# Performance work log

Measured on AMD Instinct MI355X. Metric: run time of the kernel, lower is better.

The kernel has to match this reference:

```python
import jax, jax.numpy as jnp
import numpy as np
from jax import lax

Z_MAX = 0.3
WAVELENGTHS = jnp.array([0.65, 0.53, 0.47], jnp.float32)
LUMA = jnp.array([0.299, 0.587, 0.114], jnp.float32)


def conv2d(x, w, b):
    # x: (B,C,H,W), w: (O,I,kh,kw), SAME padding, stride 1
    y = lax.conv_general_dilated(x, w, (1, 1), 'SAME',
                                 dimension_numbers=('NCHW', 'OIHW', 'NCHW'))
    return y + b[None, :, None, None]


def group_norm(x, g, b, eps=1e-5):
    # GroupNorm(num_groups=1): normalize over (C,H,W) per sample
    mu = x.mean(axis=(1, 2, 3), keepdims=True)
    var = ((x - mu) ** 2).mean(axis=(1, 2, 3), keepdims=True)
    xn = (x - mu) * lax.rsqrt(var + eps)
    return xn * g[None, :, None, None] + b[None, :, None, None]


def setup_inputs() -> dict:
    key = jax.random.key(0)
    ks = jax.random.split(key, 16)
    B, C, H, W = 8, 3, 512, 512
    PH, ZH, MH = 16, 16, 32
    s = 0.1
    inp = {
        'x': jax.random.uniform(ks[0], (B, C, H, W), jnp.float32),
        'norm_g': jnp.ones((C,), jnp.float32), 'norm_b': jnp.zeros((C,), jnp.float32),
        'ph_w1': jax.random.normal(ks[1], (PH, C, 3, 3), jnp.float32) * s,
        'ph_b1': jnp.zeros((PH,), jnp.float32),
        'ph_w2': jax.random.normal(ks[2], (C, PH, 3, 3), jnp.float32) * s,
        'ph_b2': jnp.zeros((C,), jnp.float32),
        'z_w1': jax.random.normal(ks[3], (ZH, C, 3, 3), jnp.float32) * s,
        'z_b1': jnp.zeros((ZH,), jnp.float32),
        'z_w2': jax.random.normal(ks[4], (C, ZH, 3, 3), jnp.float32) * s,
        'z_b2': jnp.zeros((C,), jnp.float32),
        'freq_gain': jax.random.normal(ks[5], (C,), jnp.float32) * 0.01,
        'mix_w1': jax.random.normal(ks[6], (MH, C + 2, 3, 3), jnp.float32) * s,
        'mix_b1': jnp.zeros((MH,), jnp.float32),
        'gn1_g': jnp.ones((MH,), jnp.float32), 'gn1_b': jnp.zeros((MH,), jnp.float32),
        'mix_w2': jax.random.normal(ks[7], (MH, MH, 3, 3), jnp.float32) * s,
        'mix_b2': jnp.zeros((MH,), jnp.float32),
        'gn2_g': jnp.ones((MH,), jnp.float32), 'gn2_b': jnp.zeros((MH,), jnp.float32),
        'mix_w3': jax.random.normal(ks[8], (C, MH, 1, 1), jnp.float32) * s,
        'mix_b3': jnp.zeros((C,), jnp.float32),
        'se_w1': jax.random.normal(ks[9], (4, C), jnp.float32) * s,   # mid = max(3//4,4)=4
        'se_b1': jnp.zeros((4,), jnp.float32),
        'se_w2': jax.random.normal(ks[10], (C, 4), jnp.float32) * s,
        'se_b2': jnp.zeros((C,), jnp.float32),
        'alpha': jnp.asarray(0.3, jnp.float32),
    }
    return inp


def reference(x, norm_g, norm_b, ph_w1, ph_b1, ph_w2, ph_b2,
              z_w1, z_b1, z_w2, z_b2, freq_gain,
              mix_w1, mix_b1, gn1_g, gn1_b, mix_w2, mix_b2, gn2_g, gn2_b,
              mix_w3, mix_b3, se_w1, se_b1, se_w2, se_b2, alpha):
    B, C, H, W = x.shape
    # 1) norm
    xn = group_norm(x, norm_g, norm_b)
    # 2) phase prediction (small CNN, phi in [-pi, pi])
    h = jax.nn.silu(conv2d(xn, ph_w1, ph_b1))
    phi = jnp.tanh(conv2d(h, ph_w2, ph_b2)) * jnp.pi
    # 3) per-pixel propagation distance z in [0, z_max]
    hz = jax.nn.silu(conv2d(xn, z_w1, z_b1))
    z = jax.nn.sigmoid(conv2d(hz, z_w2, z_b2)) * Z_MAX
    # 4) complex field U0 = amp * exp(i*phi)  (amp_mode='identity')
    U0 = lax.complex(x * jnp.cos(phi), x * jnp.sin(phi))
    # 5) ASM propagation. kz = 2*pi*sqrt(1/lam^2 - fx^2 - fy^2), per-channel wavelength.
    fy = jnp.fft.fftfreq(H).astype(jnp.float32)
    fx = jnp.fft.fftfreq(W).astype(jnp.float32)
    f2 = fy[:, None] ** 2 + fx[None, :] ** 2                     # (H,W)
    inv_l2 = (1.0 / WAVELENGTHS ** 2)[:, None, None]             # (3,1,1)
    kz = 2.0 * jnp.pi * jnp.sqrt(jnp.maximum(inv_l2 - f2[None], 0.0))  # (3,H,W)
    # spatially varying z: base propagation at mean z + spatial phase correction
    z_mean = z.mean(axis=(2, 3), keepdims=True)                  # (B,3,1,1)
    Uf = jnp.fft.fft2(U0)
    Uf = Uf * (1.0 + freq_gain)[None, :, None, None].astype(Uf.dtype)  # FreqEnhance gain
    hp = kz[None] * z_mean                                       # (B,3,H,W)
    Uz = jnp.fft.ifft2(Uf * lax.complex(jnp.cos(hp), jnp.sin(hp)))
    k0 = (2.0 * jnp.pi / WAVELENGTHS)[None, :, None, None]
    cp = k0 * (z - z_mean)
    Uz = Uz * lax.complex(jnp.cos(cp), jnp.sin(cp))
    # 6) J = |Uz| with clamped sqrt
    J = jnp.sqrt(jnp.maximum(Uz.real ** 2 + Uz.imag ** 2, 1e-12))
    # 7) mix head: [x, J_luma, J_contrast] -> delta
    lw = LUMA[None, :, None, None]
    x_l = (x * lw).sum(axis=1, keepdims=True)
    J_l = (J * lw).sum(axis=1, keepdims=True)
    mix_in = jnp.concatenate([x, J_l, J_l - x_l], axis=1)        # (B,5,H,W)
    d = jax.nn.silu(group_norm(conv2d(mix_in, mix_w1, mix_b1), gn1_g, gn1_b))
    d = jax.nn.silu(group_norm(conv2d(d, mix_w2, mix_b2), gn2_g, gn2_b))
    delta = conv2d(d, mix_w3, mix_b3)                            # (B,3,H,W)
    # 8) SE channel attention
    p = delta.mean(axis=(2, 3))                                  # (B,3)
    wse = jax.nn.sigmoid(jax.nn.silu(p @ se_w1.T + se_b1) @ se_w2.T + se_b2)
    delta = delta * wse[:, :, None, None]
    # 9) residual update
    return x + alpha * delta
```

## Files before the change

### kernel.cpp

```cpp
#include <hip/hip_runtime.h>
#include <hip/hip_bf16.h>
#include <math.h>

#define DINL __device__ __forceinline__

namespace {
constexpr int Bn = 8, Cn = 3, Hn = 512, Wn = 512;
constexpr int HW  = Hn * Wn;
constexpr int CHW = Cn * HW;
constexpr float GEPS = 1e-5f;
constexpr float PIf  = 3.14159265358979323846f;

constexpr size_t OFF_RED = 0;
constexpr size_t OFF_PHI = 512;
constexpr size_t OFF_U   = OFF_PHI + (size_t)Bn * CHW * 2;
constexpr size_t OFF_J   = OFF_U   + (size_t)Bn * CHW * 4;
constexpr size_t OFF_D   = OFF_J   + (size_t)Bn * CHW * 2;
constexpr size_t OFF_Y2  = OFF_D   + (size_t)Bn * CHW * 2;
constexpr size_t OFF_W1B = OFF_Y2  + (size_t)Bn * 32 * HW;
constexpr size_t OFF_W2F = OFF_W1B + 3072 * 2;
constexpr size_t OFF_WH1 = OFF_W2F + 9216;
constexpr size_t OFF_WP2 = OFF_WH1 + 4608 * 2;
constexpr size_t OFF_WZ2 = OFF_WP2 + 4608;
constexpr size_t OFF_PRM = OFF_WZ2 + 4608;
constexpr size_t OFF_PART= OFF_PRM + 160 * 4;
constexpr int PZ = 0;
constexpr int PG1 = 24576;
constexpr int PG2 = 40960;
constexpr int PD  = 57344;
}

typedef __bf16 bfx8 __attribute__((ext_vector_type(8)));
typedef float  fx4  __attribute__((ext_vector_type(4)));

DINL float frcp(float a) { return __builtin_amdgcn_rcpf(a); }
DINL float sigm(float a) { return frcp(1.f + __expf(-a)); }
DINL float siluf(float a) { return a * frcp(1.f + __expf(-a)); }
DINL float ftanh(float a) { return 1.f - 2.f * frcp(1.f + __expf(2.f * a)); }
DINL unsigned short f2bf(float f) {
    unsigned u = __float_as_uint(f);
    return (unsigned short)((u + 0x7FFFu + ((u >> 16) & 1u)) >> 16);
}
DINL float bf2f(unsigned short h) {
    return __uint_as_float(((unsigned)h) << 16);
}
DINL unsigned short t1(float a) { return (unsigned short)(__float_as_uint(a) >> 16); }
DINL unsigned t2(float a, float b) {
    return (__float_as_uint(a) >> 16) | (__float_as_uint(b) & 0xFFFF0000u);
}
DINL unsigned char f2f8(float v) {
    return (unsigned char)(__builtin_amdgcn_cvt_pk_fp8_f32(v, v, 0, false) & 0xFF);
}
DINL unsigned short pk8(float a, float b) {
    return (unsigned short)(__builtin_amdgcn_cvt_pk_fp8_f32(a, b, 0, false) & 0xFFFF);
}
template<int SEL>
DINL float f8f(unsigned u) { return __builtin_amdgcn_cvt_f32_fp8(u, SEL); }
DINL unsigned pkh(float a, float b) {
    auto h = __builtin_amdgcn_cvt_pkrtz(a, b);
    unsigned u; __builtin_memcpy(&u, &h, 4); return u;
}
DINL float2 uph(unsigned u) {
    _Float16 h[2]; __builtin_memcpy(h, &u, 4);
    return make_float2((float)h[0], (float)h[1]);
}
DINL unsigned short f2h(float a) {
    _Float16 h = (_Float16)a; unsigned short s; __builtin_memcpy(&s, &h, 2); return s;
}
DINL float h2f(unsigned short s) {
    _Float16 h; __builtin_memcpy(&h, &s, 2); return (float)h;
}

DINL float blockReduceSum(float v) {
    __shared__ float sm[4];
    int lane = threadIdx.x & 63, wid = threadIdx.x >> 6;
    #pragma unroll
    for (int o = 32; o > 0; o >>= 1) v += __shfl_down(v, o, 64);
    __syncthreads();
    if (lane == 0) sm[wid] = v;
    __syncthreads();
    if (wid == 0) {
        float r = (lane < 4) ? sm[lane] : 0.f;
        r += __shfl_down(r, 2, 64);
        r += __shfl_down(r, 1, 64);
        return r;
    }
    return 0.f;
}

__global__ void k_zero(float* __restrict__ red) { red[threadIdx.x] = 0.f; }

__global__ __launch_bounds__(256) void k_red(const float* __restrict__ src,
                                             float* __restrict__ dst)
{
    const float4* s4 = (const float4*)(src + (size_t)blockIdx.x * 1024);
    float4 q = s4[threadIdx.x];
    float r = blockReduceSum(q.x + q.y + q.z + q.w);
    if (threadIdx.x == 0) dst[blockIdx.x] = r;
}

__global__ __launch_bounds__(256) void k_prep(
    const float* __restrict__ w1, const float* __restrict__ w2,
    const float* __restrict__ phw1, const float* __restrict__ zw1,
    const float* __restrict__ phw2, const float* __restrict__ zw2,
    const float* __restrict__ g2g, const float* __restrict__ g2b,
    const float* __restrict__ w3,
    unsigned short* __restrict__ w1bf, unsigned char* __restrict__ w2f8,
    unsigned short* __restrict__ wh1, unsigned char* __restrict__ wp2,
    unsigned char* __restrict__ wz2, float* __restrict__ prm)
{
    int i = blockIdx.x * 256 + threadIdx.x;
    if (i < 3072) {
        int o = i / 96, k = i - o * 96;
        int ky = k >> 5, r = k & 31, kx = r >> 3, c = r & 7;
        float v = (kx < 3 && c < 5) ? w1[o * 45 + c * 9 + ky * 3 + kx] : 0.f;
        w1bf[i] = f2bf(v);
    }
    if (i < 9216) {
        int tap = i >> 10, rr = i & 1023, o = rr >> 5, ci = rr & 31;
        w2f8[i] = f2f8(w2[o * 288 + ci * 9 + tap]);
    }
    if (i < 4608) {
        int o = i / 96, k = i - o * 96;
        int ky = k >> 5, r = k & 31, kx = r >> 3, c = r & 7;
        float v = 0.f;
        if (kx < 3 && c < 3)
            v = (o < 16) ? phw1[o * 27 + c * 9 + ky * 3 + kx]
                         : zw1[(o - 16) * 27 + c * 9 + ky * 3 + kx];
        wh1[i] = f2bf(v);
    }
    if (i < 4608) {
        int tap = i / 512, rr = i - tap * 512, n = rr >> 5, k = rr & 31;
        float vp = (n < 3 && k < 16) ? phw2[n * 144 + k * 9 + tap] : 0.f;
        float vz = (n < 3) ? zw2[n * 288 + k * 9 + tap] : 0.f;
        wp2[i] = f2f8(vp);
        wz2[i] = f2f8(vz);
    }
    if (i < 160) {
        if (i < 32) {
            int ch = (i & 1) * 16 + (i >> 1);
            prm[i] = g2g[ch];
        } else if (i < 64) {
            int j = i - 32, ch = (j & 1) * 16 + (j >> 1);
            prm[i] = g2b[ch];
        } else {
            int j = (i - 64) & 31, c = (i - 64) >> 5;
            int ch = (j & 1) * 16 + (j >> 1);
            prm[i] = w3[c * 32 + ch];
        }
    }
}

__global__ __launch_bounds__(256) void k_reduce_x(const float* __restrict__ x,
                                                  float* __restrict__ red) {
    int b = blockIdx.x >> 5, blk = blockIdx.x & 31;
    const float4* xv = (const float4*)(x + (size_t)b * CHW + (size_t)blk * (CHW / 32));
    float s = 0.f, ss = 0.f;
    for (int i = threadIdx.x; i < (CHW / 32) / 4; i += 256) {
        float4 v = xv[i];
        s  += v.x + v.y + v.z + v.w;
        ss += v.x * v.x + v.y * v.y + v.z * v.z + v.w * v.w;
    }
    float rs = blockReduceSum(s);
    float rss = blockReduceSum(ss);
    if (threadIdx.x == 0) { atomicAdd(&red[b], rs); atomicAdd(&red[8 + b], rss); }
}

__global__ __launch_bounds__(256) void k_heads(
    const float* __restrict__ x, const float* __restrict__ red,
    const float* __restrict__ ng, const float* __restrict__ nb,
    const unsigned short* __restrict__ wh1,
    const float* __restrict__ phb1, const float* __restrict__ zb1,
    const unsigned char* __restrict__ wp2, const unsigned char* __restrict__ wz2,
    const float* __restrict__ phb2, const float* __restrict__ zb2,
    unsigned short* __restrict__ phi, float* __restrict__ part)
{
    const int tx0 = blockIdx.x * 16, ty0 = blockIdx.y * 16, b = blockIdx.z;
    const int local = blockIdx.y * 32 + blockIdx.x;
    const bool edge = (blockIdx.x == 0) || (blockIdx.x == 31) ||
                      (blockIdx.y == 0) || (blockIdx.y == 31);
    __shared__ unsigned short mt8[20 * 21 * 8];
    __shared__ __attribute__((aligned(16))) unsigned char ht8[324 * 48];
    const int t = threadIdx.x;
    const float mu = red[b] * (1.f / CHW);
    const float rsv = rsqrtf(red[8 + b] * (1.f / CHW) - mu * mu + GEPS);
    float sc[3], sh[3];
    #pragma unroll
    for (int c = 0; c < 3; ++c) { sc[c] = rsv * ng[c]; sh[c] = nb[c] - mu * rsv * ng[c]; }
    if (edge) {
        for (int e = t; e < 20 * 21; e += 256) {
            int yy = e / 21, xx = e - yy * 21;
            int gy = ty0 - 2 + yy, gx = tx0 - 2 + xx;
            float v0 = 0, v1 = 0, v2 = 0;
            if (xx < 20 && (unsigned)gy < (unsigned)Hn && (unsigned)gx < (unsigned)Wn) {
                size_t p = (size_t)b * CHW + (size_t)gy * Wn + gx;
                v0 = x[p] * sc[0] + sh[0];
                v1 = x[p + HW] * sc[1] + sh[1];
                v2 = x[p + 2 * HW] * sc[2] + sh[2];
            }
            *(uint4*)(mt8 + e * 8) = make_uint4(t2(v0, v1), (unsigned)t1(v2), 0u, 0u);
        }
    } else {
        for (int e = t; e < 20 * 21; e += 256) {
            int yy = e / 21, xx = e - yy * 21;
            float v0 = 0, v1 = 0, v2 = 0;
            if (xx < 20) {
                size_t p = (size_t)b * CHW + (size_t)(ty0 - 2 + yy) * Wn + (tx0 - 2 + xx);
                v0 = x[p] * sc[0] + sh[0];
                v1 = x[p + HW] * sc[1] + sh[1];
                v2 = x[p + 2 * HW] * sc[2] + sh[2];
            }
            *(uint4*)(mt8 + e * 8) = make_uint4(t2(v0, v1), (unsigned)t1(v2), 0u, 0u);
        }
    }
    const int wv = t >> 6, lane = t & 63, ln = lane & 15, q = lane >> 4;
    bfx8 Bf[3][3];
    #pragma unroll
    for (int ks = 0; ks < 3; ++ks)
        #pragma unroll
        for (int nt = 0; nt < 3; ++nt)
            Bf[ks][nt] = *(const bfx8*)(wh1 + (nt * 16 + ln) * 96 + ks * 32 + q * 8);
    const float bb0 = phb1[ln], bb1 = zb1[ln], bb2 = zb1[16 + ln];
    __syncthreads();
    for (int mt = wv; mt < 21; mt += 4) {
        int p = mt * 16 + ln; if (p > 323) p = 323;
        const int hy = p / 18, hx = p - hy * 18;
        fx4 a0 = {0,0,0,0}, a1 = {0,0,0,0}, a2 = {0,0,0,0};
        #pragma unroll
        for (int ks = 0; ks < 3; ++ks) {
            bfx8 A = *(const bfx8*)(mt8 + ((hy + ks) * 21 + hx + q) * 8);
            a0 = __builtin_amdgcn_mfma_f32_16x16x32_bf16(A, Bf[ks][0], a0, 0, 0, 0);
            a1 = __builtin_amdgcn_mfma_f32_16x16x32_bf16(A, Bf[ks][1], a1, 0, 0, 0);
            a2 = __builtin_amdgcn_mfma_f32_16x16x32_bf16(A, Bf[ks][2], a2, 0, 0, 0);
        }
        const int prb = mt * 16 + q * 4;
        if (edge) {
            #pragma unroll
            for (int r = 0; r < 4; ++r) {
                const int pr = prb + r;
                if (pr < 324) {
                    const int py = pr / 18, px = pr - py * 18;
                    const int gy = ty0 - 1 + py, gx = tx0 - 1 + px;
                    const bool inimg = (unsigned)gy < (unsigned)Hn && (unsigned)gx < (unsigned)Wn;
                    unsigned char* hp = ht8 + pr * 48;
                    hp[ln]      = inimg ? f2f8(siluf(a0[r] + bb0)) : (unsigned char)0;
                    hp[16 + ln] = inimg ? f2f8(siluf(a1[r] + bb1)) : (unsigned char)0;
                    hp[32 + ln] = inimg ? f2f8(siluf(a2[r] + bb2)) : (unsigned char)0;
                }
            }
        } else {
            #pragma unroll
            for (int r = 0; r < 4; ++r) {
                const int pr = prb + r;
                if (pr < 324) {
                    unsigned char* hp = ht8 + pr * 48;
                    hp[ln]      = f2f8(siluf(a0[r] + bb0));
                    hp[16 + ln] = f2f8(siluf(a1[r] + bb1));
                    hp[32 + ln] = f2f8(siluf(a2[r] + bb2));
                }
            }
        }
    }
    __syncthreads();
    fx4 accp[4], accz[4];
    #pragma unroll
    for (int i = 0; i < 4; ++i) { accp[i] = fx4{0,0,0,0}; accz[i] = fx4{0,0,0,0}; }
    #pragma unroll
    for (int tap = 0; tap < 9; ++tap) {
        const int ky = tap / 3, kx = tap - ky * 3;
        long Bp = *(const long*)(wp2 + tap * 512 + ln * 32 + q * 8);
        long Bz = *(const long*)(wz2 + tap * 512 + ln * 32 + q * 8);
        #pragma unroll
        for (int i = 0; i < 4; ++i) {
            const int oy = wv * 4 + i;
            const unsigned char* ap = ht8 + ((oy + ky) * 18 + ln + kx) * 48;
            long Ap = *(const long*)(ap + q * 8);
            long Az = *(const long*)(ap + 16 + q * 8);
            accp[i] = __builtin_amdgcn_mfma_f32_16x16x32_fp8_fp8(Ap, Bp, accp[i], 0, 0, 0);
            accz[i] = __builtin_amdgcn_mfma_f32_16x16x32_fp8_fp8(Az, Bz, accz[i], 0, 0, 0);
        }
    }
    __syncthreads();
    float* phs = (float*)ht8;
    float* zs  = phs + 1024;
    if (ln < 3) {
        #pragma unroll
        for (int i = 0; i < 4; ++i)
            #pragma unroll
            for (int r = 0; r < 4; ++r) {
                int pl = (wv * 4 + i) * 16 + q * 4 + r;
                phs[pl * 4 + ln] = accp[i][r];
                zs [pl * 4 + ln] = accz[i][r];
            }
    }
    asm volatile("" ::: "memory");
    float4 pv = ((const float4*)phs)[t];
    float4 zv = ((const float4*)zs)[t];
    const int gy = ty0 + (t >> 4), gx = tx0 + (t & 15);
    size_t pp = (size_t)b * CHW + (size_t)gy * Wn + gx;
    phi[pp]          = f2h(ftanh(pv.x + phb2[0]) * PIf);
    phi[pp + HW]     = f2h(ftanh(pv.y + phb2[1]) * PIf);
    phi[pp + 2 * HW] = f2h(ftanh(pv.z + phb2[2]) * PIf);
    float z0 = sigm(zv.x + zb2[0]) * 0.3f;
    float z1 = sigm(zv.y + zb2[1]) * 0.3f;
    float z2 = sigm(zv.z + zb2[2]) * 0.3f;
    float r0 = blockReduceSum(z0);
    float r1 = blockReduceSum(z1);
    float r2 = blockReduceSum(z2);
    if (t == 0) {
        part[PZ + (size_t)(b * 3 + 0) * 1024 + local] = r0;
        part[PZ + (size_t)(b * 3 + 1) * 1024 + local] = r1;
        part[PZ + (size_t)(b * 3 + 2) * 1024 + local] = r2;
    }
}

template<bool INV>
DINL float2* fft512_wave4(float2* a, float2* b, const float2* tw, int l)
{
    float2* src = a; float2* dst = b;
    int s = 1;
    #pragma unroll
    for (int st = 0; st < 4; ++st) {
        #pragma unroll
        for (int h = 0; h < 2; ++h) {
            const int i = l + h * 64;
            const int q = i & (s - 1);
            const int sm = i - q;
            float2 A = src[i], B = src[i + 128], C = src[i + 256], D = src[i + 384];
            float t0x = A.x + C.x, t0y = A.y + C.y;
            float t1x = A.x - C.x, t1y = A.y - C.y;
            float t2x = B.x + D.x, t2y = B.y + D.y;
            float t3x = B.x - D.x, t3y = B.y - D.y;
            float i3x = INV ? -t3y : t3y;
            float i3y = INV ? t3x : -t3x;
            float u0x = t0x + t2x, u0y = t0y + t2y;
            float u2x = t0x - t2x, u2y = t0y - t2y;
            float u1x = t1x + i3x, u1y = t1y + i3y;
            float u3x = t1x - i3x, u3y = t1y - i3y;
            float2 w1 = tw[sm], w2 = tw[2 * sm], w3 = tw[3 * sm];
            float w1y = INV ? -w1.y : w1.y;
            float w2y = INV ? -w2.y : w2.y;
            float w3y = INV ? -w3.y : w3.y;
            const int base = q + 4 * sm;
            dst[base]         = make_float2(u0x, u0y);
            dst[base + s]     = make_float2(u1x * w1.x - u1y * w1y, u1x * w1y + u1y * w1.x);
            dst[base + 2 * s] = make_float2(u2x * w2.x - u2y * w2y, u2x * w2y + u2y * w2.x);
            dst[base + 3 * s] = make_float2(u3x * w3.x - u3y * w3y, u3x * w3y + u3y * w3.x);
        }
        float2* tmp = src; src = dst; dst = tmp;
        s <<= 2;
        asm volatile("" ::: "memory");
    }
    #pragma unroll
    for (int h = 0; h < 4; ++h) {
        const int j = l + h * 64;
        float2 u = src[j], v = src[j + 256];
        dst[j]       = make_float2(u.x + v.x, u.y + v.y);
        dst[j + 256] = make_float2(u.x - v.x, u.y - v.y);
    }
    float2* tmp = src; src = dst; dst = tmp;
    asm volatile("" ::: "memory");
    return src;
}

__global__ __launch_bounds__(256) void k_fftA(
    const float* __restrict__ x, const unsigned short* __restrict__ phi,
    unsigned* __restrict__ U)
{
    __shared__ float2 buf[4][2][512];
    __shared__ float2 tw[512];
    const int t = threadIdx.x, wv = t >> 6, l = t & 63;
    #pragma unroll
    for (int i = t; i < 512; i += 256) {
        float s, c; __sincosf(-2.f * PIf * (float)i * (1.f / 512.f), &s, &c);
        tw[i] = make_float2(c, s);
    }
    __syncthreads();
    const size_t line = (size_t)blockIdx.x * 4 + wv;
    const float* xr = x + line * 512;
    const unsigned short* pr = phi + line * 512;
    float2* A = buf[wv][0];
    float2* B = buf[wv][1];
    #pragma unroll
    for (int i = l; i < 512; i += 64) {
        float s, c; __sincosf(h2f(pr[i]), &s, &c);
        float xv = xr[i];
        A[i] = make_float2(xv * c, xv * s);
    }
    asm volatile("" ::: "memory");
    float2* res = fft512_wave4<false>(A, B, tw, l);
    unsigned* Ur = U + line * 512;
    #pragma unroll
    for (int i = l; i < 512; i += 64) Ur[i] = pkh(res[i].x, res[i].y);
}

__global__ __launch_bounds__(256) void k_transpose(unsigned* __restrict__ U)
{
    const int img = blockIdx.y;
    int rem = blockIdx.x, ti = 0;
    while (rem >= 16 - ti) { rem -= 16 - ti; ++ti; }
    const int tj = ti + rem;
    unsigned* Ub = U + (size_t)img * HW;
    __shared__ unsigned ta[32][33];
    __shared__ unsigned tb[32][33];
    const int t = threadIdx.x;
    const int cc = t & 31, r0 = t >> 5;
    const int ar = ti * 32, ac = tj * 32;
    #pragma unroll
    for (int k = 0; k < 4; ++k) {
        int r = r0 + k * 8;
        ta[r][cc] = Ub[(size_t)(ar + r) * 512 + ac + cc];
    }
    if (ti != tj) {
        #pragma unroll
        for (int k = 0; k < 4; ++k) {
            int r = r0 + k * 8;
            tb[r][cc] = Ub[(size_t)(ac + r) * 512 + ar + cc];
        }
    }
    __syncthreads();
    #pragma unroll
    for (int k = 0; k < 4; ++k) {
        int r = r0 + k * 8;
        Ub[(size_t)(ac + r) * 512 + ar + cc] = ta[cc][r];
    }
    if (ti != tj) {
        #pragma unroll
        for (int k = 0; k < 4; ++k) {
            int r = r0 + k * 8;
            Ub[(size_t)(ar + r) * 512 + ac + cc] = tb[cc][r];
        }
    }
}

__global__ __launch_bounds__(256) void k_fftB(
    unsigned* __restrict__ U, const float* __restrict__ red, const float* __restrict__ fgain)
{
    __shared__ float2 buf[4][2][512];
    __shared__ float2 tw[512];
    const int t = threadIdx.x, wv = t >> 6, l = t & 63;
    #pragma unroll
    for (int i = t; i < 512; i += 256) {
        float s, c; __sincosf(-2.f * PIf * (float)i * (1.f / 512.f), &s, &c);
        tw[i] = make_float2(c, s);
    }
    __syncthreads();
    const int line = blockIdx.x * 4 + wv;
    const int bc = line >> 9;
    const int fw = line & 511;
    const int c = bc % 3;
    unsigned* Ur = U + (size_t)line * 512;
    float2* A = buf[wv][0];
    float2* B = buf[wv][1];
    #pragma unroll
    for (int i = l; i < 512; i += 64) A[i] = uph(Ur[i]);
    asm volatile("" ::: "memory");
    float2* res = fft512_wave4<false>(A, B, tw, l);
    const float zm   = red[16 + bc] * (1.f / HW);
    const float gain = 1.f + fgain[c];
    const float lam  = (c == 0) ? 0.65f : (c == 1) ? 0.53f : 0.47f;
    const float il2  = 1.f / (lam * lam);
    const float fwv  = (float)(fw < 256 ? fw : fw - 512) * (1.f / 512.f);
    const float f2w  = fwv * fwv;
    #pragma unroll
    for (int i = l; i < 512; i += 64) {
        float fh = (float)(i < 256 ? i : i - 512) * (1.f / 512.f);
        float kz = 2.f * PIf * sqrtf(fmaxf(il2 - f2w - fh * fh, 0.f));
        float sn, cs; __sincosf(kz * zm, &sn, &cs);
        float2 v = res[i];
        res[i] = make_float2(gain * (v.x * cs - v.y * sn), gain * (v.x * sn + v.y * cs));
    }
    asm volatile("" ::: "memory");
    float2* other = (res == A) ? B : A;
    float2* res2 = fft512_wave4<true>(res, other, tw, l);
    #pragma unroll
    for (int i = l; i < 512; i += 64) {
        float2 v = res2[i];
        Ur[i] = pkh(v.x * (1.f / 512.f), v.y * (1.f / 512.f));
    }
}

__global__ __launch_bounds__(256) void k_fftC(
    const unsigned* __restrict__ U, unsigned short* __restrict__ J)
{
    __shared__ float2 buf[4][2][512];
    __shared__ float2 tw[512];
    const int t = threadIdx.x, wv = t >> 6, l = t & 63;
    #pragma unroll
    for (int i = t; i < 512; i += 256) {
        float s, c; __sincosf(-2.f * PIf * (float)i * (1.f / 512.f), &s, &c);
        tw[i] = make_float2(c, s);
    }
    __syncthreads();
    const size_t line = (size_t)blockIdx.x * 4 + wv;
    const unsigned* Ur = U + line * 512;
    float2* A = buf[wv][0];
    float2* B = buf[wv][1];
    #pragma unroll
    for (int i = l; i < 512; i += 64) A[i] = uph(Ur[i]);
    asm volatile("" ::: "memory");
    float2* res = fft512_wave4<true>(A, B, tw, l);
    unsigned short* Jr = J + line * 512;
    #pragma unroll
    for (int i = l; i < 512; i += 64) {
        float2 v = res[i];
        float re = v.x * (1.f / 512.f), im = v.y * (1.f / 512.f);
        Jr[i] = f2h(sqrtf(fmaxf(re * re + im * im, 1e-12f)));
    }
}

__global__ __launch_bounds__(256) void k_m1(
    const float* __restrict__ x, const unsigned short* __restrict__ Jb,
    const unsigned short* __restrict__ w1bf, const float* __restrict__ b1,
    float* __restrict__ part)
{
    const int tx0 = blockIdx.x * 16, ty0 = blockIdx.y * 16, b = blockIdx.z;
    const int local = blockIdx.y * 32 + blockIdx.x;
    const bool edge = (blockIdx.x == 0) || (blockIdx.x == 31) ||
                      (blockIdx.y == 0) || (blockIdx.y == 31);
    __shared__ unsigned short mt8[18 * 19 * 8];
    const int t = threadIdx.x;
    for (int e = t; e < 18 * 19; e += 256) {
        int yy = e / 19, xx = e - yy * 19;
        int gy = ty0 - 1 + yy, gx = tx0 - 1 + xx;
        float v0 = 0, v1 = 0, v2 = 0, jl = 0, d5 = 0;
        bool ok = edge ? (xx < 18 && (unsigned)gy < (unsigned)Hn && (unsigned)gx < (unsigned)Wn)
                       : (xx < 18);
        if (ok) {
            size_t p = (size_t)b * CHW + (size_t)gy * Wn + gx;
            v0 = x[p]; v1 = x[p + HW]; v2 = x[p + 2 * HW];
            float j0 = h2f(Jb[p]), j1 = h2f(Jb[p + HW]), j2 = h2f(Jb[p + 2 * HW]);
            float xl = 0.299f * v0 + 0.587f * v1 + 0.114f * v2;
            jl = 0.299f * j0 + 0.587f * j1 + 0.114f * j2;
            d5 = jl - xl;
        }
        *(uint4*)(mt8 + e * 8) = make_uint4(t2(v0, v1), t2(v2, jl), (unsigned)t1(d5), 0u);
    }
    __syncthreads();
    const int wv = t >> 6, lane = t & 63, ln = lane & 15, q = lane >> 4;
    bfx8 Bf[3][2];
    #pragma unroll
    for (int ks = 0; ks < 3; ++ks)
        #pragma unroll
        for (int nt = 0; nt < 2; ++nt)
            Bf[ks][nt] = *(const bfx8*)(w1bf + (nt * 16 + ln) * 96 + ks * 32 + q * 8);
    const float b1v0 = b1[ln], b1v1 = b1[16 + ln];
    float s = 0.f, ss = 0.f;
    #pragma unroll
    for (int i = 0; i < 4; ++i) {
        const int oy = wv * 4 + i;
        fx4 a0 = {0.f, 0.f, 0.f, 0.f}, a1 = {0.f, 0.f, 0.f, 0.f};
        #pragma unroll
        for (int ks = 0; ks < 3; ++ks) {
            bfx8 A = *(const bfx8*)(mt8 + ((oy + ks) * 19 + ln + q) * 8);
            a0 = __builtin_amdgcn_mfma_f32_16x16x32_bf16(A, Bf[ks][0], a0, 0, 0, 0);
            a1 = __builtin_amdgcn_mfma_f32_16x16x32_bf16(A, Bf[ks][1], a1, 0, 0, 0);
        }
        #pragma unroll
        for (int r = 0; r < 4; ++r) {
            float u0 = a0[r] + b1v0, u1 = a1[r] + b1v1;
            s += u0 + u1; ss += u0 * u0 + u1 * u1;
        }
    }
    float rs = blockReduceSum(s);
    float rss = blockReduceSum(ss);
    if (t == 0) {
        part[PG1 + (size_t)b * 1024 + local] = rs;
        part[PG1 + (size_t)(8 + b) * 1024 + local] = rss;
    }
}

__global__ __launch_bounds__(256) void k_m2(
    const float* __restrict__ x, const unsigned short* __restrict__ Jb,
    const unsigned short* __restrict__ w1bf, const float* __restrict__ b1,
    const float* __restrict__ g1g, const float* __restrict__ g1b,
    const unsigned char* __restrict__ w2f8, const float* __restrict__ b2,
    const float* __restrict__ red, float* __restrict__ part,
    unsigned char* __restrict__ y2)
{
    const int tx0 = blockIdx.x * 16, ty0 = blockIdx.y * 16, b = blockIdx.z;
    const int local = blockIdx.y * 32 + blockIdx.x;
    const bool edge = (blockIdx.x == 0) || (blockIdx.x == 31) ||
                      (blockIdx.y == 0) || (blockIdx.y == 31);
    __shared__ unsigned short mt8[20 * 21 * 8];
    __shared__ __attribute__((aligned(16))) unsigned char dt2[324 * 40];
    const int t = threadIdx.x;
    const float mu1 = red[40 + b] * (1.f / (32.f * HW));
    const float rs1 = rsqrtf(red[48 + b] * (1.f / (32.f * HW)) - mu1 * mu1 + GEPS);
    for (int e = t; e < 20 * 21; e += 256) {
        int yy = e / 21, xx = e - yy * 21;
        int gy = ty0 - 2 + yy, gx = tx0 - 2 + xx;
        float v0 = 0, v1 = 0, v2 = 0, jl = 0, d5 = 0;
        bool ok = edge ? (xx < 20 && (unsigned)gy < (unsigned)Hn && (unsigned)gx < (unsigned)Wn)
                       : (xx < 20);
        if (ok) {
            size_t p = (size_t)b * CHW + (size_t)gy * Wn + gx;
            v0 = x[p]; v1 = x[p + HW]; v2 = x[p + 2 * HW];
            float j0 = h2f(Jb[p]), j1 = h2f(Jb[p + HW]), j2 = h2f(Jb[p + 2 * HW]);
            float xl = 0.299f * v0 + 0.587f * v1 + 0.114f * v2;
            jl = 0.299f * j0 + 0.587f * j1 + 0.114f * j2;
            d5 = jl - xl;
        }
        *(uint4*)(mt8 + e * 8) = make_uint4(t2(v0, v1), t2(v2, jl), (unsigned)t1(d5), 0u);
    }
    const int wv = t >> 6, lane = t & 63, ln = lane & 15, q = lane >> 4;
    const float sc0 = rs1 * g1g[ln],       sc1 = rs1 * g1g[16 + ln];
    const float of0 = (b1[ln] - mu1) * sc0 + g1b[ln];
    const float of1 = (b1[16 + ln] - mu1) * sc1 + g1b[16 + ln];
    bfx8 Bf[3][2];
    #pragma unroll
    for (int ks = 0; ks < 3; ++ks)
        #pragma unroll
        for (int nt = 0; nt < 2; ++nt)
            Bf[ks][nt] = *(const bfx8*)(w1bf + (nt * 16 + ln) * 96 + ks * 32 + q * 8);
    __syncthreads();
    for (int mt = wv; mt < 21; mt += 4) {
        int p = mt * 16 + ln; if (p > 323) p = 323;
        const int hy = p / 18, hx = p - hy * 18;
        fx4 a0 = {0.f, 0.f, 0.f, 0.f}, a1 = {0.f, 0.f, 0.f, 0.f};
        #pragma unroll
        for (int ks = 0; ks < 3; ++ks) {
            bfx8 A = *(const bfx8*)(mt8 + ((hy + ks) * 21 + hx + q) * 8);
            a0 = __builtin_amdgcn_mfma_f32_16x16x32_bf16(A, Bf[ks][0], a0, 0, 0, 0);
            a1 = __builtin_amdgcn_mfma_f32_16x16x32_bf16(A, Bf[ks][1], a1, 0, 0, 0);
        }
        const int prb = mt * 16 + q * 4;
        if (edge) {
            #pragma unroll
            for (int r = 0; r < 4; ++r) {
                const int pr = prb + r;
                if (pr < 324) {
                    const int py = pr / 18, px = pr - py * 18;
                    const int gy = ty0 - 1 + py, gx = tx0 - 1 + px;
                    const bool inimg = (unsigned)gy < (unsigned)Hn && (unsigned)gx < (unsigned)Wn;
                    dt2[pr * 40 + ln]      = inimg ? f2f8(siluf(a0[r] * sc0 + of0)) : (unsigned char)0;
                    dt2[pr * 40 + 16 + ln] = inimg ? f2f8(siluf(a1[r] * sc1 + of1)) : (unsigned char)0;
                }
            }
        } else {
            #pragma unroll
            for (int r = 0; r < 4; ++r) {
                const int pr = prb + r;
                if (pr < 324) {
                    dt2[pr * 40 + ln]      = f2f8(siluf(a0[r] * sc0 + of0));
                    dt2[pr * 40 + 16 + ln] = f2f8(siluf(a1[r] * sc1 + of1));
                }
            }
        }
    }
    __syncthreads();
    fx4 c2[4][2];
    #pragma unroll
    for (int i = 0; i < 4; ++i)
        #pragma unroll
        for (int nt = 0; nt < 2; ++nt)
            c2[i][nt] = fx4{0.f, 0.f, 0.f, 0.f};
    #pragma unroll
    for (int tap = 0; tap < 9; ++tap) {
        const int ky = tap / 3, kx = tap - ky * 3;
        long B0 = *(const long*)(w2f8 + tap * 1024 + ln * 32 + q * 8);
        long B1 = *(const long*)(w2f8 + tap * 1024 + (16 + ln) * 32 + q * 8);
        #pragma unroll
        for (int i = 0; i < 4; ++i) {
            const int oy = wv * 4 + i;
            long A = *(const long*)(dt2 + ((oy + ky) * 18 + ln + kx) * 40 + q * 8);
            c2[i][0] = __builtin_amdgcn_mfma_f32_16x16x32_fp8_fp8(A, B0, c2[i][0], 0, 0, 0);
            c2[i][1] = __builtin_amdgcn_mfma_f32_16x16x32_fp8_fp8(A, B1, c2[i][1], 0, 0, 0);
        }
    }
    float s = 0.f, ss = 0.f;
    const float b2v0 = b2[ln], b2v1 = b2[16 + ln];
    #pragma unroll
    for (int i = 0; i < 4; ++i) {
        const int gy = ty0 + wv * 4 + i;
        #pragma unroll
        for (int r = 0; r < 4; ++r) {
            const int gx = tx0 + q * 4 + r;
            float a0 = c2[i][0][r] + b2v0;
            float a1 = c2[i][1][r] + b2v1;
            s += a0 + a1; ss += a0 * a0 + a1 * a1;
            size_t off = ((size_t)b * HW + (size_t)gy * Wn + gx) * 32 + ln * 2;
            *(unsigned short*)(y2 + off) = pk8(a0, a1);
        }
    }
    float rsum = blockReduceSum(s);
    float rss = blockReduceSum(ss);
    if (t == 0) {
        part[PG2 + (size_t)b * 1024 + local] = rsum;
        part[PG2 + (size_t)(8 + b) * 1024 + local] = rss;
    }
}

__global__ __launch_bounds__(256) void k_m3(
    const unsigned char* __restrict__ y2, const float* __restrict__ red,
    const float* __restrict__ prm, const float* __restrict__ b3,
    unsigned short* __restrict__ dl, float* __restrict__ part)
{
    int idx = blockIdx.x * 256 + threadIdx.x;
    int b = idx >> 18;
    int pix = idx & (HW - 1);
    const int local = blockIdx.x & 1023;
    float mu = red[56 + b] * (1.f / (32.f * HW));
    float rs = rsqrtf(red[64 + b] * (1.f / (32.f * HW)) - mu * mu + GEPS);
    const uint4* yp = (const uint4*)(y2 + (size_t)idx * 32);
    uint4 L0 = yp[0], L1 = yp[1];
    unsigned Lw[8] = {L0.x, L0.y, L0.z, L0.w, L1.x, L1.y, L1.z, L1.w};
    float a0 = b3[0], a1 = b3[1], a2 = b3[2];
    #pragma unroll
    for (int w = 0; w < 8; ++w) {
        unsigned u = Lw[w];
        float vv[4] = { f8f<0>(u), f8f<1>(u), f8f<2>(u), f8f<3>(u) };
        #pragma unroll
        for (int h = 0; h < 4; ++h) {
            int j = w * 4 + h;
            float dn = (vv[h] - mu) * rs * prm[j] + prm[32 + j];
            float sv = siluf(dn);
            a0 += sv * prm[64 + j]; a1 += sv * prm[96 + j]; a2 += sv * prm[128 + j];
        }
    }
    size_t p = (size_t)b * CHW + pix;
    dl[p] = f2h(a0); dl[p + HW] = f2h(a1); dl[p + 2 * HW] = f2h(a2);
    float r0 = blockReduceSum(a0);
    float r1 = blockReduceSum(a1);
    float r2 = blockReduceSum(a2);
    if (threadIdx.x == 0) {
        part[PD + (size_t)(b * 3 + 0) * 1024 + local] = r0;
        part[PD + (size_t)(b * 3 + 1) * 1024 + local] = r1;
        part[PD + (size_t)(b * 3 + 2) * 1024 + local] = r2;
    }
}

__global__ void k_se(float* __restrict__ red,
    const float* __restrict__ w1, const float* __restrict__ b1,
    const float* __restrict__ w2, const float* __restrict__ b2,
    const float* __restrict__ alpha)
{
    int b = threadIdx.x;
    if (b < 8) {
        float p0 = red[72 + b * 3 + 0] * (1.f / HW);
        float p1 = red[72 + b * 3 + 1] * (1.f / HW);
        float p2 = red[72 + b * 3 + 2] * (1.f / HW);
        float h[4];
        #pragma unroll
        for (int j = 0; j < 4; ++j) {
            float a = b1[j] + p0 * w1[j * 3] + p1 * w1[j * 3 + 1] + p2 * w1[j * 3 + 2];
            h[j] = siluf(a);
        }
        float al = alpha[0];
        #pragma unroll
        for (int c = 0; c < 3; ++c) {
            float a = b2[c] + h[0] * w2[c * 4] + h[1] * w2[c * 4 + 1]
                            + h[2] * w2[c * 4 + 2] + h[3] * w2[c * 4 + 3];
            red[96 + b * 3 + c] = al * sigm(a);
        }
    }
}

__global__ __launch_bounds__(256) void k_out(
    const float* __restrict__ x, const unsigned short* __restrict__ dl,
    const float* __restrict__ red, float* __restrict__ out)
{
    int i = blockIdx.x * 256 + threadIdx.x;
    float aw = red[96 + (i >> 16)];
    float4 xv = ((const float4*)x)[i];
    uint2 dv2 = ((const uint2*)dl)[i];
    float2 d01 = uph(dv2.x);
    float2 d23 = uph(dv2.y);
    float4 o;
    o.x = xv.x + aw * d01.x; o.y = xv.y + aw * d01.y;
    o.z = xv.z + aw * d23.x; o.w = xv.w + aw * d23.y;
    ((float4*)out)[i] = o;
}

extern "C" void kernel_launch(void* const* d_in, const int* in_sizes, int n_in,
                              void* d_out, int out_size, void* d_ws, size_t ws_size,
                              hipStream_t stream)
{
    const float* x     = (const float*)d_in[0];
    const float* ng    = (const float*)d_in[1];
    const float* nb    = (const float*)d_in[2];
    const float* ph_w1 = (const float*)d_in[3];
    const float* ph_b1 = (const float*)d_in[4];
    const float* ph_w2 = (const float*)d_in[5];
    const float* ph_b2 = (const float*)d_in[6];
    const float* z_w1  = (const float*)d_in[7];
    const float* z_b1  = (const float*)d_in[8];
    const float* z_w2  = (const float*)d_in[9];
    const float* z_b2  = (const float*)d_in[10];
    const float* fgain = (const float*)d_in[11];
    const float* mw1   = (const float*)d_in[12];
    const float* mb1   = (const float*)d_in[13];
    const float* g1g   = (const float*)d_in[14];
    const float* g1b   = (const float*)d_in[15];
    const float* mw2   = (const float*)d_in[16];
    const float* mb2   = (const float*)d_in[17];
    const float* g2g   = (const float*)d_in[18];
    const float* g2b   = (const float*)d_in[19];
    const float* mw3   = (const float*)d_in[20];
    const float* mb3   = (const float*)d_in[21];
    const float* sw1   = (const float*)d_in[22];
    const float* sb1   = (const float*)d_in[23];
    const float* sw2   = (const float*)d_in[24];
    const float* sb2   = (const float*)d_in[25];
    const float* alpha = (const float*)d_in[26];

    char* ws = (char*)d_ws;
    float*  red = (float*)(ws + OFF_RED);
    unsigned short* phi = (unsigned short*)(ws + OFF_PHI);
    unsigned* U = (unsigned*)(ws + OFF_U);
    unsigned short* Jb = (unsigned short*)(ws + OFF_J);
    unsigned short* dl = (unsigned short*)(ws + OFF_D);
    unsigned char*  y2   = (unsigned char*)(ws + OFF_Y2);
    unsigned short* w1bf = (unsigned short*)(ws + OFF_W1B);
    unsigned char*  w2f8 = (unsigned char*)(ws + OFF_W2F);
    unsigned short* wh1  = (unsigned short*)(ws + OFF_WH1);
    unsigned char*  wp2  = (unsigned char*)(ws + OFF_WP2);
    unsigned char*  wz2  = (unsigned char*)(ws + OFF_WZ2);
    float* prm  = (float*)(ws + OFF_PRM);
    float* part = (float*)(ws + OFF_PART);
    float* out = (float*)d_out;

    hipLaunchKernelGGL(k_zero, dim3(1), dim3(128), 0, stream, red);
    hipLaunchKernelGGL(k_prep, dim3(36), dim3(256), 0, stream,
                       mw1, mw2, ph_w1, z_w1, ph_w2, z_w2, g2g, g2b, mw3,
                       w1bf, w2f8, wh1, wp2, wz2, prm);
    hipLaunchKernelGGL(k_reduce_x, dim3(256), dim3(256), 0, stream, x, red);
    hipLaunchKernelGGL(k_heads, dim3(32, 32, 8), dim3(256), 0, stream,
                       x, red, ng, nb, wh1, ph_b1, z_b1, wp2, wz2, ph_b2, z_b2, phi, part);
    hipLaunchKernelGGL(k_red, dim3(24), dim3(256), 0, stream, part + PZ, red + 16);
    hipLaunchKernelGGL(k_fftA, dim3(3072), dim3(256), 0, stream, x, phi, U);
    hipLaunchKernelGGL(k_transpose, dim3(136, 24), dim3(256), 0, stream, U);
    hipLaunchKernelGGL(k_fftB, dim3(3072), dim3(256), 0, stream, U, red, fgain);
    hipLaunchKernelGGL(k_transpose, dim3(136, 24), dim3(256), 0, stream, U);
    hipLaunchKernelGGL(k_fftC, dim3(3072), dim3(256), 0, stream, U, Jb);
    hipLaunchKernelGGL(k_m1, dim3(32, 32, 8), dim3(256), 0, stream, x, Jb, w1bf, mb1, part);
    hipLaunchKernelGGL(k_red, dim3(16), dim3(256), 0, stream, part + PG1, red + 40);
    hipLaunchKernelGGL(k_m2, dim3(32, 32, 8), dim3(256), 0, stream,
                       x, Jb, w1bf, mb1, g1g, g1b, w2f8, mb2, red, part, y2);
    hipLaunchKernelGGL(k_red, dim3(16), dim3(256), 0, stream, part + PG2, red + 56);
    hipLaunchKernelGGL(k_m3, dim3(8192), dim3(256), 0, stream, y2, red, prm, mb3, dl, part);
    hipLaunchKernelGGL(k_red, dim3(24), dim3(256), 0, stream, part + PD, red + 72);
    hipLaunchKernelGGL(k_se, dim3(1), dim3(64), 0, stream, red, sw1, sb1, sw2, sb2, alpha);
    hipLaunchKernelGGL(k_out, dim3(6144), dim3(256), 0, stream, x, dl, red, out);
}
```

Measured before the change: 499.4 us.

## Use K=128 scaled FP8 MFMA for 3x3 conv taps and fold small kernels

Packs four 3x3 taps into the K dimension so that the second-layer convolutions in k_heads and k_m2 can use the 16x16x128 f8f6f4 MFMA. This replaces nine K=32 MFMAs per row with two K=128 MFMAs plus one K=32 MFMA for the last tap, and adds repacked weight buffers built in k_prep. The dt2 row stride grows from 40 to 48 bytes so that 32-byte vector loads from LDS work. It also folds zeroing of the reduction buffer into k_prep and the final delta reduction into k_se, which removes two kernel launches. The per-row LDS reads of 32 contiguous bytes assume the activation layout lines up with the tap-major K packing; the wider stride adds LDS usage and may cause bank conflicts.

After: 521.9 us. 4.5% more time.

```diff
diff --git a/kernel.cpp b/kernel.cpp
--- a/kernel.cpp
+++ b/kernel.cpp
@@ -23,7 +23,10 @@
 constexpr size_t OFF_WP2 = OFF_WH1 + 4608 * 2;
 constexpr size_t OFF_WZ2 = OFF_WP2 + 4608;
 constexpr size_t OFF_PRM = OFF_WZ2 + 4608;
-constexpr size_t OFF_PART= OFF_PRM + 160 * 4;
+constexpr size_t OFF_WPS = OFF_PRM + 160 * 4;
+constexpr size_t OFF_WZS = OFF_WPS + 4096;
+constexpr size_t OFF_WMS = OFF_WZS + 4096;
+constexpr size_t OFF_PART= OFF_WMS + 8192;
 constexpr int PZ = 0;
 constexpr int PG1 = 24576;
 constexpr int PG2 = 40960;
@@ -32,6 +35,7 @@
 
 typedef __bf16 bfx8 __attribute__((ext_vector_type(8)));
 typedef float  fx4  __attribute__((ext_vector_type(4)));
+typedef int    ix8  __attribute__((ext_vector_type(8)));
 
 DINL float frcp(float a) { return __builtin_amdgcn_rcpf(a); }
 DINL float sigm(float a) { return frcp(1.f + __expf(-a)); }
@@ -70,6 +74,10 @@
 DINL float h2f(unsigned short s) {
     _Float16 h; __builtin_memcpy(&h, &s, 2); return (float)h;
 }
+DINL fx4 mfma128(ix8 a, ix8 b, fx4 c) {
+    return __builtin_amdgcn_mfma_scale_f32_16x16x128_f8f6f4(
+        a, b, c, 0, 0, 0, 0x7F7F7F7F, 0, 0x7F7F7F7F);
+}
 
 DINL float blockReduceSum(float v) {
     __shared__ float sm[4];
@@ -87,8 +95,6 @@
     }
     return 0.f;
 }
-
-__global__ void k_zero(float* __restrict__ red) { red[threadIdx.x] = 0.f; }
 
 __global__ __launch_bounds__(256) void k_red(const float* __restrict__ src,
                                              float* __restrict__ dst)
@@ -107,9 +113,12 @@
     const float* __restrict__ w3,
     unsigned short* __restrict__ w1bf, unsigned char* __restrict__ w2f8,
     unsigned short* __restrict__ wh1, unsigned char* __restrict__ wp2,
-    unsigned char* __restrict__ wz2, float* __restrict__ prm)
+    unsigned char* __restrict__ wz2, float* __restrict__ prm,
+    unsigned char* __restrict__ wps, unsigned char* __restrict__ wzs,
+    unsigned char* __restrict__ wms, float* __restrict__ red)
 {
     int i = blockIdx.x * 256 + threadIdx.x;
+    if (blockIdx.x == 0 && threadIdx.x < 128) red[threadIdx.x] = 0.f;
     if (i < 3072) {
         int o = i / 96, k = i - o * 96;
         int ky = k >> 5, r = k & 31, kx = r >> 3, c = r & 7;
@@ -135,6 +144,19 @@
         float vz = (n < 3) ? zw2[n * 288 + k * 9 + tap] : 0.f;
         wp2[i] = f2f8(vp);
         wz2[i] = f2f8(vz);
+    }
+    if (i < 4096) {
+        int g = i >> 11, rr = i & 2047, n = rr >> 7, k = rr & 127;
+        int tl = k >> 5, kk = k & 31, tap = g * 4 + tl;
+        float vp = (n < 3 && kk < 16) ? phw2[n * 144 + kk * 9 + tap] : 0.f;
+        float vz = (n < 3) ? zw2[n * 288 + kk * 9 + tap] : 0.f;
+        wps[i] = f2f8(vp);
+        wzs[i] = f2f8(vz);
+    }
+    if (i < 8192) {
+        int g = i >> 12, rr = i & 4095, o = rr >> 7, k = rr & 127;
+        int tl = k >> 5, kk = k & 31, tap = g * 4 + tl;
+        wms[i] = f2f8(w2[o * 288 + kk * 9 + tap]);
     }
     if (i < 160) {
         if (i < 32) {
@@ -172,6 +194,7 @@
     const unsigned short* __restrict__ wh1,
     const float* __restrict__ phb1, const float* __restrict__ zb1,
     const unsigned char* __restrict__ wp2, const unsigned char* __restrict__ wz2,
+    const unsigned char* __restrict__ wps, const unsigned char* __restrict__ wzs,
     const float* __restrict__ phb2, const float* __restrict__ zb2,
     unsigned short* __restrict__ phi, float* __restrict__ part)
 {
@@ -262,23 +285,33 @@
         }
     }
     __syncthreads();
+    const int ky0 = (q >= 3) ? 1 : 0, kx0 = (q < 3) ? q : 0;
+    const int tq1 = 4 + q;
+    const int ky1 = (tq1 < 6) ? 1 : 2, kx1 = (tq1 < 6) ? (tq1 - 3) : (tq1 - 6);
+    ix8 Bp0 = *(const ix8*)(wps + ln * 128 + q * 32);
+    ix8 Bp1 = *(const ix8*)(wps + 2048 + ln * 128 + q * 32);
+    ix8 Bz0 = *(const ix8*)(wzs + ln * 128 + q * 32);
+    ix8 Bz1 = *(const ix8*)(wzs + 2048 + ln * 128 + q * 32);
+    long Bp8 = *(const long*)(wp2 + 8 * 512 + ln * 32 + q * 8);
+    long Bz8 = *(const long*)(wz2 + 8 * 512 + ln * 32 + q * 8);
     fx4 accp[4], accz[4];
     #pragma unroll
     for (int i = 0; i < 4; ++i) { accp[i] = fx4{0,0,0,0}; accz[i] = fx4{0,0,0,0}; }
     #pragma unroll
-    for (int tap = 0; tap < 9; ++tap) {
-        const int ky = tap / 3, kx = tap - ky * 3;
-        long Bp = *(const long*)(wp2 + tap * 512 + ln * 32 + q * 8);
-        long Bz = *(const long*)(wz2 + tap * 512 + ln * 32 + q * 8);
-        #pragma unroll
-        for (int i = 0; i < 4; ++i) {
-            const int oy = wv * 4 + i;
-            const unsigned char* ap = ht8 + ((oy + ky) * 18 + ln + kx) * 48;
-            long Ap = *(const long*)(ap + q * 8);
-            long Az = *(const long*)(ap + 16 + q * 8);
-            accp[i] = __builtin_amdgcn_mfma_f32_16x16x32_fp8_fp8(Ap, Bp, accp[i], 0, 0, 0);
-            accz[i] = __builtin_amdgcn_mfma_f32_16x16x32_fp8_fp8(Az, Bz, accz[i], 0, 0, 0);
-        }
+    for (int i = 0; i < 4; ++i) {
+        const int oy = wv * 4 + i;
+        const unsigned char* r0 = ht8 + ((oy + ky0) * 18 + ln + kx0) * 48;
+        const unsigned char* r1 = ht8 + ((oy + ky1) * 18 + ln + kx1) * 48;
+        const unsigned char* r8 = ht8 + ((oy + 2) * 18 + ln + 2) * 48;
+        ix8 Ap0 = *(const ix8*)r0, Az0 = *(const ix8*)(r0 + 16);
+        ix8 Ap1 = *(const ix8*)r1, Az1 = *(const ix8*)(r1 + 16);
+        long A8p = *(const long*)(r8 + q * 8), A8z = *(const long*)(r8 + 16 + q * 8);
+        accp[i] = mfma128(Ap0, Bp0, accp[i]);
+        accz[i] = mfma128(Az0, Bz0, accz[i]);
+        accp[i] = mfma128(Ap1, Bp1, accp[i]);
+        accz[i] = mfma128(Az1, Bz1, accz[i]);
+        accp[i] = __builtin_amdgcn_mfma_f32_16x16x32_fp8_fp8(A8p, Bp8, accp[i], 0, 0, 0);
+        accz[i] = __builtin_amdgcn_mfma_f32_16x16x32_fp8_fp8(A8z, Bz8, accz[i], 0, 0, 0);
     }
     __syncthreads();
     float* phs = (float*)ht8;
@@ -574,7 +607,8 @@
     const float* __restrict__ x, const unsigned short* __restrict__ Jb,
     const unsigned short* __restrict__ w1bf, const float* __restrict__ b1,
     const float* __restrict__ g1g, const float* __restrict__ g1b,
-    const unsigned char* __restrict__ w2f8, const float* __restrict__ b2,
+    const unsigned char* __restrict__ w2f8, const unsigned char* __restrict__ wms,
+    const float* __restrict__ b2,
     const float* __restrict__ red, float* __restrict__ part,
     unsigned char* __restrict__ y2)
 {
@@ -583,7 +617,7 @@
     const bool edge = (blockIdx.x == 0) || (blockIdx.x == 31) ||
                       (blockIdx.y == 0) || (blockIdx.y == 31);
     __shared__ unsigned short mt8[20 * 21 * 8];
-    __shared__ __attribute__((aligned(16))) unsigned char dt2[324 * 40];
+    __shared__ __attribute__((aligned(16))) unsigned char dt2[324 * 48];
     const int t = threadIdx.x;
     const float mu1 = red[40 + b] * (1.f / (32.f * HW));
     const float rs1 = rsqrtf(red[48 + b] * (1.f / (32.f * HW)) - mu1 * mu1 + GEPS);
@@ -633,8 +667,8 @@
                     const int py = pr / 18, px = pr - py * 18;
                     const int gy = ty0 - 1 + py, gx = tx0 - 1 + px;
                     const bool inimg = (unsigned)gy < (unsigned)Hn && (unsigned)gx < (unsigned)Wn;
-                    dt2[pr * 40 + ln]      = inimg ? f2f8(siluf(a0[r] * sc0 + of0)) : (unsigned char)0;
-                    dt2[pr * 40 + 16 + ln] = inimg ? f2f8(siluf(a1[r] * sc1 + of1)) : (unsigned char)0;
+                    dt2[pr * 48 + ln]      = inimg ? f2f8(siluf(a0[r] * sc0 + of0)) : (unsigned char)0;
+                    dt2[pr * 48 + 16 + ln] = inimg ? f2f8(siluf(a1[r] * sc1 + of1)) : (unsigned char)0;
                 }
             }
         } else {
@@ -642,13 +676,22 @@
             for (int r = 0; r < 4; ++r) {
                 const int pr = prb + r;
                 if (pr < 324) {
-                    dt2[pr * 40 + ln]      = f2f8(siluf(a0[r] * sc0 + of0));
-                    dt2[pr * 40 + 16 + ln] = f2f8(siluf(a1[r] * sc1 + of1));
+                    dt2[pr * 48 + ln]      = f2f8(siluf(a0[r] * sc0 + of0));
+                    dt2[pr * 48 + 16 + ln] = f2f8(siluf(a1[r] * sc1 + of1));
                 }
             }
         }
     }
     __syncthreads();
+    const int ky0 = (q >= 3) ? 1 : 0, kx0 = (q < 3) ? q : 0;
+    const int tq1 = 4 + q;
+    const int ky1 = (tq1 < 6) ? 1 : 2, kx1 = (tq1 < 6) ? (tq1 - 3) : (tq1 - 6);
+    ix8 Bm00 = *(const ix8*)(wms + ln * 128 + q * 32);
+    ix8 Bm01 = *(const ix8*)(wms + (16 + ln) * 128 + q * 32);
+    ix8 Bm10 = *(const ix8*)(wms + 4096 + ln * 128 + q * 32);
+    ix8 Bm11 = *(const ix8*)(wms + 4096 + (16 + ln) * 128 + q * 32);
+    long B80 = *(const long*)(w2f8 + 8 * 1024 + ln * 32 + q * 8);
+    long B81 = *(const long*)(w2f8 + 8 * 1024 + (16 + ln) * 32 + q * 8);
     fx4 c2[4][2];
     #pragma unroll
     for (int i = 0; i < 4; ++i)
@@ -656,17 +699,20 @@
         for (int nt = 0; nt < 2; ++nt)
             c2[i][nt] = fx4{0.f, 0.f, 0.f, 0.f};
     #pragma unroll
-    for (int tap = 0; tap < 9; ++tap) {
-        const int ky = tap / 3, kx = tap - ky * 3;
-        long B0 = *(const long*)(w2f8 + tap * 1024 + ln * 32 + q * 8);
-        long B1 = *(const long*)(w2f8 + tap * 1024 + (16 + ln) * 32 + q * 8);
-        #pragma unroll
-        for (int i = 0; i < 4; ++i) {
-            const int oy = wv * 4 + i;
-            long A = *(const long*)(dt2 + ((oy + ky) * 18 + ln + kx) * 40 + q * 8);
-            c2[i][0] = __builtin_amdgcn_mfma_f32_16x16x32_fp8_fp8(A, B0, c2[i][0], 0, 0, 0);
-            c2[i][1] = __builtin_amdgcn_mfma_f32_16x16x32_fp8_fp8(A, B1, c2[i][1], 0, 0, 0);
-        }
+    for (int i = 0; i < 4; ++i) {
+        const int oy = wv * 4 + i;
+        const unsigned char* r0 = dt2 + ((oy + ky0) * 18 + ln + kx0) * 48;
+        const unsigned char* r1 = dt2 + ((oy + ky1) * 18 + ln + kx1) * 48;
+        const unsigned char* r8 = dt2 + ((oy + 2) * 18 + ln + 2) * 48;
+        ix8 A0 = *(const ix8*)r0;
+        ix8 A1 = *(const ix8*)r1;
+        long A8 = *(const long*)(r8 + q * 8);
+        c2[i][0] = mfma128(A0, Bm00, c2[i][0]);
+        c2[i][1] = mfma128(A0, Bm01, c2[i][1]);
+        c2[i][0] = mfma128(A1, Bm10, c2[i][0]);
+        c2[i][1] = mfma128(A1, Bm11, c2[i][1]);
+        c2[i][0] = __builtin_amdgcn_mfma_f32_16x16x32_fp8_fp8(A8, B80, c2[i][0], 0, 0, 0);
+        c2[i][1] = __builtin_amdgcn_mfma_f32_16x16x32_fp8_fp8(A8, B81, c2[i][1], 0, 0, 0);
     }
     float s = 0.f, ss = 0.f;
     const float b2v0 = b2[ln], b2v1 = b2[16 + ln];
@@ -730,16 +776,26 @@
     }
 }
 
-__global__ void k_se(float* __restrict__ red,
+__global__ __launch_bounds__(256) void k_se(const float* __restrict__ part,
+    float* __restrict__ red,
     const float* __restrict__ w1, const float* __restrict__ b1,
     const float* __restrict__ w2, const float* __restrict__ b2,
     const float* __restrict__ alpha)
 {
-    int b = threadIdx.x;
+    __shared__ float ds[24];
+    const int t = threadIdx.x;
+    for (int g = 0; g < 24; ++g) {
+        const float4* s4 = (const float4*)(part + PD + (size_t)g * 1024);
+        float4 qv = s4[t];
+        float r = blockReduceSum(qv.x + qv.y + qv.z + qv.w);
+        if (t == 0) ds[g] = r;
+    }
+    __syncthreads();
+    int b = t;
     if (b < 8) {
-        float p0 = red[72 + b * 3 + 0] * (1.f / HW);
-        float p1 = red[72 + b * 3 + 1] * (1.f / HW);
-        float p2 = red[72 + b * 3 + 2] * (1.f / HW);
+        float p0 = ds[b * 3 + 0] * (1.f / HW);
+        float p1 = ds[b * 3 + 1] * (1.f / HW);
+        float p2 = ds[b * 3 + 2] * (1.f / HW);
         float h[4];
         #pragma unroll
         for (int j = 0; j < 4; ++j) {
@@ -817,16 +873,19 @@
     unsigned char*  wp2  = (unsigned char*)(ws + OFF_WP2);
     unsigned char*  wz2  = (unsigned char*)(ws + OFF_WZ2);
     float* prm  = (float*)(ws + OFF_PRM);
+    unsigned char*  wps  = (unsigned char*)(ws + OFF_WPS);
+    unsigned char*  wzs  = (unsigned char*)(ws + OFF_WZS);
+    unsigned char*  wms  = (unsigned char*)(ws + OFF_WMS);
     float* part = (float*)(ws + OFF_PART);
     float* out = (float*)d_out;
 
-    hipLaunchKernelGGL(k_zero, dim3(1), dim3(128), 0, stream, red);
     hipLaunchKernelGGL(k_prep, dim3(36), dim3(256), 0, stream,
                        mw1, mw2, ph_w1, z_w1, ph_w2, z_w2, g2g, g2b, mw3,
-                       w1bf, w2f8, wh1, wp2, wz2, prm);
+                       w1bf, w2f8, wh1, wp2, wz2, prm, wps, wzs, wms, red);
     hipLaunchKernelGGL(k_reduce_x, dim3(256), dim3(256), 0, stream, x, red);
     hipLaunchKernelGGL(k_heads, dim3(32, 32, 8), dim3(256), 0, stream,
-                       x, red, ng, nb, wh1, ph_b1, z_b1, wp2, wz2, ph_b2, z_b2, phi, part);
+                       x, red, ng, nb, wh1, ph_b1, z_b1, wp2, wz2, wps, wzs,
+                       ph_b2, z_b2, phi, part);
     hipLaunchKernelGGL(k_red, dim3(24), dim3(256), 0, stream, part + PZ, red + 16);
     hipLaunchKernelGGL(k_fftA, dim3(3072), dim3(256), 0, stream, x, phi, U);
     hipLaunchKernelGGL(k_transpose, dim3(136, 24), dim3(256), 0, stream, U);
@@ -836,10 +895,9 @@
     hipLaunchKernelGGL(k_m1, dim3(32, 32, 8), dim3(256), 0, stream, x, Jb, w1bf, mb1, part);
     hipLaunchKernelGGL(k_red, dim3(16), dim3(256), 0, stream, part + PG1, red + 40);
     hipLaunchKernelGGL(k_m2, dim3(32, 32, 8), dim3(256), 0, stream,
-                       x, Jb, w1bf, mb1, g1g, g1b, w2f8, mb2, red, part, y2);
+                       x, Jb, w1bf, mb1, g1g, g1b, w2f8, wms, mb2, red, part, y2);
     hipLaunchKernelGGL(k_red, dim3(16), dim3(256), 0, stream, part + PG2, red + 56);
     hipLaunchKernelGGL(k_m3, dim3(8192), dim3(256), 0, stream, y2, red, prm, mb3, dl, part);
-    hipLaunchKernelGGL(k_red, dim3(24), dim3(256), 0, stream, part + PD, red + 72);
-    hipLaunchKernelGGL(k_se, dim3(1), dim3(64), 0, stream, red, sw1, sb1, sw2, sb2, alpha);
+    hipLaunchKernelGGL(k_se, dim3(1), dim3(256), 0, stream, part, red, sw1, sb1, sw2, sb2, alpha);
     hipLaunchKernelGGL(k_out, dim3(6144), dim3(256), 0, stream, x, dl, red, out);
 }
```
